# Kernel optimization log

Measured on AMD Instinct MI355X. Metric: run time of the kernel, lower is better.

## Reference

```python
import jax, jax.numpy as jnp
import numpy as np

DIM = 256
B, N, M = 4, 4096, 8


def setup_inputs() -> dict:
    key = jax.random.key(0)
    ks = jax.random.split(key, 12)
    s = 1.0 / np.sqrt(DIM)
    return {
        "q": jax.random.normal(ks[0], (B, DIM, N, M), jnp.float32),
        "k": jax.random.normal(ks[1], (B, DIM, N, M), jnp.float32),
        "pos": jax.random.normal(ks[2], (B, N, M, DIM), jnp.float32),
        "mask": jnp.ones((B, N, M, 1), jnp.int32),
        "Wq": jax.random.normal(ks[3], (DIM, DIM), jnp.float32) * s,
        "Wk": jax.random.normal(ks[4], (DIM, DIM), jnp.float32) * s,
        "Wv": jax.random.normal(ks[5], (DIM, DIM), jnp.float32) * s,
        "W1": jax.random.normal(ks[6], (DIM, DIM // 2), jnp.float32) * s,
        "b1": jnp.zeros((DIM // 2,), jnp.float32),
        "W2": jax.random.normal(ks[7], (DIM // 2, DIM), jnp.float32) * s,
        "b2": jnp.zeros((DIM,), jnp.float32),
        "Wo": jax.random.normal(ks[8], (DIM, DIM), jnp.float32) * s,
        "bo": jnp.zeros((DIM,), jnp.float32),
    }


def reference(q, k, pos, mask, Wq, Wk, Wv, W1, b1, W2, b2, Wo, bo):
    # (B, dim, N, M) -> (B, N, M, dim)
    qh = jnp.einsum('bdnm,de->bnme', q, Wq)
    kh = jnp.einsum('bdnm,de->bnme', k, Wk)
    v = kh @ Wv  # note: v_fc applied to k_fc output, as in the original
    attn = kh - qh + pos
    attn = jax.nn.relu(attn @ W1 + b1) @ W2 + b2
    attn = jnp.where(mask == 0, -1e9, attn)
    attn = jax.nn.sigmoid(attn)
    x = (v + pos) * attn
    x = x @ Wo + bo
    return jnp.transpose(x, (0, 3, 1, 2))  # back to (B, dim, N, M)
```

## Files before the change

kernel.cpp:

```cpp
#include <hip/hip_runtime.h>

#define DIMX 256
#define NMX  32768
#define TB   64
#define PITCH 544

typedef short s16x8 __attribute__((ext_vector_type(8)));
typedef float f32x4 __attribute__((ext_vector_type(4)));

#define OFF_WQN   (0u)
#define OFF_WK    (131072u)
#define OFF_WKV   (262144u)
#define OFF_W1    (393216u)
#define OFF_W2    (458752u)
#define OFF_WO    (524288u)
#define OFF_KVF32 (655360u)

__device__ __forceinline__ ushort f2bf(float f) {
  uint u = __builtin_bit_cast(uint, f);
  return (ushort)((u + 0x7FFFu + ((u >> 16) & 1u)) >> 16);
}

__device__ __forceinline__ uint cvtpk(float lo, float hi) {
  uint r;
  asm("v_cvt_pk_bf16_f32 %0, %1, %2" : "=v"(r) : "v"(lo), "v"(hi));
  return r;
}
__device__ __forceinline__ float bf_lo(uint u) {
  return __builtin_bit_cast(float, u << 16);
}
__device__ __forceinline__ float bf_hi(uint u) {
  return __builtin_bit_cast(float, u & 0xffff0000u);
}

__global__ void wkv_kernel(const float* __restrict__ Wk, const float* __restrict__ Wv,
                           float* __restrict__ outw) {
  const int e = threadIdx.x, d = blockIdx.x;
  float acc = 0.f;
  #pragma unroll 8
  for (int m = 0; m < DIMX; ++m) acc += Wk[d * DIMX + m] * Wv[m * DIMX + e];
  outw[d * DIMX + e] = acc;
}

__global__ void pack_kernel(const float* __restrict__ Wq, const float* __restrict__ Wk,
                            const float* __restrict__ Wkvf, const float* __restrict__ W1,
                            const float* __restrict__ W2, const float* __restrict__ Wo,
                            ushort* __restrict__ wsout) {
  const int fid = blockIdx.x, lane = threadIdx.x;
  const float* src; int Eout = 256; float sgn = 1.f; uint off; int local;
  if (fid < 128)      { src = Wq;   sgn = -1.f; off = OFF_WQN; local = fid;       }
  else if (fid < 256) { src = Wk;   off = OFF_WK;  local = fid - 128;             }
  else if (fid < 384) { src = Wkvf; off = OFF_WKV; local = fid - 256;             }
  else if (fid < 448) { src = W1;   Eout = 128; off = OFF_W1; local = fid - 384;  }
  else if (fid < 512) { src = W2;   off = OFF_W2;  local = fid - 448;             }
  else                { src = Wo;   off = OFF_WO;  local = fid - 512;             }
  const int R  = Eout >> 4;
  const int ks = local / R, r = local - ks * R;
  const int e  = r * 16 + (lane & 15);
  const int k0 = ks * 32 + (lane >> 4) * 8;
  union { uint4 u4; ushort us[8]; } o;
  #pragma unroll
  for (int j = 0; j < 8; ++j) o.us[j] = f2bf(sgn * src[(k0 + j) * Eout + e]);
  *(uint4*)((char*)wsout + off + (((uint)local * 64u + (uint)lane) * 16u)) = o.u4;
}

#define MFMA16(A,B,C) __builtin_amdgcn_mfma_f32_16x16x32_bf16(A, B, C, 0, 0, 0)

__global__ __launch_bounds__(512, 4) void fused_main(
    const float* __restrict__ q, const float* __restrict__ kin,
    const float* __restrict__ pos, const int* __restrict__ mask,
    const float* __restrict__ b1, const float* __restrict__ b2,
    const float* __restrict__ bo, const ushort* __restrict__ wfr,
    float* __restrict__ out)
{
  __shared__ __align__(128) char ba[TB * PITCH];
  __shared__ __align__(128) char bb[TB * PITCH];
  const char* wb = (const char*)wfr;

  const int tid = threadIdx.x;
  const int w = tid >> 6, l = tid & 63;
  const int c = l & 15, g = l >> 4;
  const int b  = blockIdx.x >> 9;
  const int t0 = (blockIdx.x & 511) * TB;

  auto ldB = [&](const char* buf, int ks, int tf) -> s16x8 {
    const int t = (tf << 4) + c;
    const int col = (ks << 6) + (g << 4);
    return *(const s16x8*)(buf + t * PITCH + (col ^ ((t & 7) << 4)));
  };
  auto ldA = [&](uint moff, int fi) -> s16x8 {
    return *(const s16x8*)(wb + moff + (((uint)fi << 6) | (uint)l) * 16u);
  };
  auto stW4 = [&](char* buf, int e0, int t, uint lo, uint hi) {
    const int byte = t * PITCH + (((uint)(e0 * 2)) ^ ((t & 7) << 4));
    *(uint2*)(buf + byte) = uint2{lo, hi};
  };

  const size_t gbase = (size_t)b * DIMX * NMX + t0 + l;

  #pragma unroll
  for (int j4 = 0; j4 < 4; ++j4) {
    const int d0 = (w << 5) + (j4 << 3);
    uint pq[4], pk[4];
    #pragma unroll
    for (int p = 0; p < 4; ++p) {
      const size_t o0 = gbase + (size_t)(d0 + 2 * p) * NMX;
      const size_t o1 = o0 + NMX;
      pq[p] = cvtpk(__builtin_nontemporal_load(q + o0),
                    __builtin_nontemporal_load(q + o1));
      pk[p] = cvtpk(__builtin_nontemporal_load(kin + o0),
                    __builtin_nontemporal_load(kin + o1));
    }
    const int byte = l * PITCH + ((d0 << 1) ^ ((l & 7) << 4));
    *(uint4*)(ba + byte) = uint4{pq[0], pq[1], pq[2], pq[3]};
    *(uint4*)(bb + byte) = uint4{pk[0], pk[1], pk[2], pk[3]};
  }

  f32x4 posr[4][2];
  {
    const float* pz = pos + ((size_t)b * NMX + t0) * DIMX;
    #pragma unroll
    for (int tf = 0; tf < 4; ++tf) {
      const int t = (tf << 4) + c;
      #pragma unroll
      for (int ef = 0; ef < 2; ++ef) {
        const int e0 = (w << 5) + (ef << 4) + (g << 2);
        posr[tf][ef] =
            __builtin_nontemporal_load((const f32x4*)(pz + (size_t)t * DIMX + e0));
      }
    }
  }
  int mk[4];
  #pragma unroll
  for (int tf = 0; tf < 4; ++tf)
    mk[tf] = mask[(size_t)b * NMX + t0 + (tf << 4) + c];

  __syncthreads();

  uint posbf[2][4][2];
  #pragma unroll
  for (int tf = 0; tf < 4; ++tf)
    #pragma unroll
    for (int ef = 0; ef < 2; ++ef) {
      posbf[ef][tf][0] = cvtpk(posr[tf][ef][0], posr[tf][ef][1]);
      posbf[ef][tf][1] = cvtpk(posr[tf][ef][2], posr[tf][ef][3]);
    }

  f32x4 av[2][4], aa[2][4];
  #pragma unroll
  for (int ef = 0; ef < 2; ++ef)
    #pragma unroll
    for (int tf = 0; tf < 4; ++tf) {
      av[ef][tf] = f32x4{0.f, 0.f, 0.f, 0.f};
      aa[ef][tf] = f32x4{0.f, 0.f, 0.f, 0.f};
    }
  #pragma unroll 2
  for (int ks = 0; ks < 8; ++ks) {
    const s16x8 v0 = ldA(OFF_WKV, (ks << 4) + (w << 1));
    const s16x8 v1 = ldA(OFF_WKV, (ks << 4) + (w << 1) + 1);
    const s16x8 k0 = ldA(OFF_WK,  (ks << 4) + (w << 1));
    const s16x8 k1 = ldA(OFF_WK,  (ks << 4) + (w << 1) + 1);
    #pragma unroll
    for (int tf = 0; tf < 4; ++tf) {
      const s16x8 bf = ldB(bb, ks, tf);
      av[0][tf] = MFMA16(v0, bf, av[0][tf]);
      av[1][tf] = MFMA16(v1, bf, av[1][tf]);
      aa[0][tf] = MFMA16(k0, bf, aa[0][tf]);
      aa[1][tf] = MFMA16(k1, bf, aa[1][tf]);
    }
  }
  uint vbf[2][4][2];
  #pragma unroll
  for (int ef = 0; ef < 2; ++ef)
    #pragma unroll
    for (int tf = 0; tf < 4; ++tf) {
      vbf[ef][tf][0] = cvtpk(av[ef][tf][0], av[ef][tf][1]);
      vbf[ef][tf][1] = cvtpk(av[ef][tf][2], av[ef][tf][3]);
    }

  #pragma unroll 2
  for (int ks = 0; ks < 8; ++ks) {
    const s16x8 a0 = ldA(OFF_WQN, (ks << 4) + (w << 1));
    const s16x8 a1 = ldA(OFF_WQN, (ks << 4) + (w << 1) + 1);
    #pragma unroll
    for (int tf = 0; tf < 4; ++tf) {
      const s16x8 bf = ldB(ba, ks, tf);
      aa[0][tf] = MFMA16(a0, bf, aa[0][tf]);
      aa[1][tf] = MFMA16(a1, bf, aa[1][tf]);
    }
  }
  __syncthreads();

  #pragma unroll
  for (int tf = 0; tf < 4; ++tf) {
    const int t = (tf << 4) + c;
    #pragma unroll
    for (int ef = 0; ef < 2; ++ef) {
      const int e0 = (w << 5) + (ef << 4) + (g << 2);
      const uint p0 = posbf[ef][tf][0], p1 = posbf[ef][tf][1];
      const uint lo = cvtpk(aa[ef][tf][0] + bf_lo(p0), aa[ef][tf][1] + bf_hi(p0));
      const uint hi = cvtpk(aa[ef][tf][2] + bf_lo(p1), aa[ef][tf][3] + bf_hi(p1));
      stW4(ba, e0, t, lo, hi);
    }
  }
  __syncthreads();

  f32x4 ah[4];
  #pragma unroll
  for (int tf = 0; tf < 4; ++tf) ah[tf] = f32x4{0.f, 0.f, 0.f, 0.f};
  #pragma unroll 2
  for (int ks = 0; ks < 8; ++ks) {
    const s16x8 a0 = ldA(OFF_W1, (ks << 3) + w);
    #pragma unroll
    for (int tf = 0; tf < 4; ++tf) {
      const s16x8 bf = ldB(ba, ks, tf);
      ah[tf] = MFMA16(a0, bf, ah[tf]);
    }
  }
  {
    const int e0h = (w << 4) + (g << 2);
    const f32x4 b1v = *(const f32x4*)(b1 + e0h);
    #pragma unroll
    for (int tf = 0; tf < 4; ++tf) {
      const int t = (tf << 4) + c;
      const uint lo = cvtpk(fmaxf(ah[tf][0] + b1v[0], 0.f),
                            fmaxf(ah[tf][1] + b1v[1], 0.f));
      const uint hi = cvtpk(fmaxf(ah[tf][2] + b1v[2], 0.f),
                            fmaxf(ah[tf][3] + b1v[3], 0.f));
      stW4(bb, e0h, t, lo, hi);
    }
  }
  __syncthreads();

  f32x4 as_[2][4];
  #pragma unroll
  for (int ef = 0; ef < 2; ++ef)
    #pragma unroll
    for (int tf = 0; tf < 4; ++tf) as_[ef][tf] = f32x4{0.f, 0.f, 0.f, 0.f};
  #pragma unroll
  for (int ks = 0; ks < 4; ++ks) {
    const s16x8 a0 = ldA(OFF_W2, (ks << 4) + (w << 1));
    const s16x8 a1 = ldA(OFF_W2, (ks << 4) + (w << 1) + 1);
    #pragma unroll
    for (int tf = 0; tf < 4; ++tf) {
      const s16x8 bf = ldB(bb, ks, tf);
      as_[0][tf] = MFMA16(a0, bf, as_[0][tf]);
      as_[1][tf] = MFMA16(a1, bf, as_[1][tf]);
    }
  }
  #pragma unroll
  for (int tf = 0; tf < 4; ++tf) {
    const int t = (tf << 4) + c;
    #pragma unroll
    for (int ef = 0; ef < 2; ++ef) {
      const int e0 = (w << 5) + (ef << 4) + (g << 2);
      const f32x4 b2v = *(const f32x4*)(b2 + e0);
      float xv[4];
      #pragma unroll
      for (int i = 0; i < 4; ++i) {
        float sv = as_[ef][tf][i] + b2v[i];
        if (mk[tf] == 0) sv = -1e9f;
        const float sig = 1.f / (1.f + __expf(-sv));
        const uint pv = vbf[ef][tf][i >> 1];
        const uint pp = posbf[ef][tf][i >> 1];
        const float vv = (i & 1) ? bf_hi(pv) : bf_lo(pv);
        const float pf = (i & 1) ? bf_hi(pp) : bf_lo(pp);
        xv[i] = (vv + pf) * sig;
      }
      stW4(ba, e0, t, cvtpk(xv[0], xv[1]), cvtpk(xv[2], xv[3]));
    }
  }
  __syncthreads();

  f32x4 ao[2][4];
  #pragma unroll
  for (int ef = 0; ef < 2; ++ef)
    #pragma unroll
    for (int tf = 0; tf < 4; ++tf) ao[ef][tf] = f32x4{0.f, 0.f, 0.f, 0.f};
  #pragma unroll 2
  for (int ks = 0; ks < 8; ++ks) {
    const s16x8 a0 = ldA(OFF_WO, (ks << 4) + (w << 1));
    const s16x8 a1 = ldA(OFF_WO, (ks << 4) + (w << 1) + 1);
    #pragma unroll
    for (int tf = 0; tf < 4; ++tf) {
      const s16x8 bf = ldB(ba, ks, tf);
      ao[0][tf] = MFMA16(a0, bf, ao[0][tf]);
      ao[1][tf] = MFMA16(a1, bf, ao[1][tf]);
    }
  }
  #pragma unroll
  for (int ef = 0; ef < 2; ++ef) {
    const int e0 = (w << 5) + (ef << 4) + (g << 2);
    const f32x4 bov = *(const f32x4*)(bo + e0);
    #pragma unroll
    for (int i = 0; i < 4; ++i) {
      float* ob = out + ((size_t)b * DIMX + e0 + i) * NMX + t0 + c;
      #pragma unroll
      for (int tf = 0; tf < 4; ++tf)
        ob[tf << 4] = ao[ef][tf][i] + bov[i];
    }
  }
}

extern "C" void kernel_launch(void* const* d_in, const int* in_sizes, int n_in,
                              void* d_out, int out_size, void* d_ws, size_t ws_size,
                              hipStream_t stream) {
  (void)in_sizes; (void)n_in; (void)out_size; (void)ws_size;
  const float* q   = (const float*)d_in[0];
  const float* k   = (const float*)d_in[1];
  const float* pos = (const float*)d_in[2];
  const int*   msk = (const int*)d_in[3];
  const float* Wq  = (const float*)d_in[4];
  const float* Wk  = (const float*)d_in[5];
  const float* Wv  = (const float*)d_in[6];
  const float* W1  = (const float*)d_in[7];
  const float* b1  = (const float*)d_in[8];
  const float* W2  = (const float*)d_in[9];
  const float* b2  = (const float*)d_in[10];
  const float* Wo  = (const float*)d_in[11];
  const float* bo  = (const float*)d_in[12];
  float* out = (float*)d_out;
  char* ws = (char*)d_ws;
  float*  wkvf = (float*)(ws + OFF_KVF32);
  ushort* wfr  = (ushort*)ws;

  wkv_kernel<<<dim3(256), dim3(256), 0, stream>>>(Wk, Wv, wkvf);
  pack_kernel<<<dim3(640), dim3(64), 0, stream>>>(Wq, Wk, wkvf, W1, W2, Wo, wfr);
  fused_main<<<dim3(2048), dim3(512), 0, stream>>>(q, k, pos, msk, b1, b2, bo, wfr, out);
}
```

Measured before the change: 180.7 us.

## Shrink LDS by staging q in two halves through a half-width buffer

Replaces the second full-width LDS tile with a half-width one (APITCH 288) so the block's shared memory drops from about 68KB to about 53KB. The q tile is loaded in two halves: the upper half is held in registers, written into the small buffer after the first half's MFMAs, and consumed in a second K loop. The W1 hidden output (128 wide) also reuses the small buffer. The launch-bounds min-blocks hint rises from 4 to 6 to allow more resident blocks, at the cost of an extra barrier, extra live registers for the held q values, and tighter register limits.

```diff
diff --git a/kernel.cpp b/kernel.cpp
--- a/kernel.cpp
+++ b/kernel.cpp
@@ -4,6 +4,7 @@
 #define NMX  32768
 #define TB   64
 #define PITCH 544
+#define APITCH 288
 
 typedef short s16x8 __attribute__((ext_vector_type(8)));
 typedef float f32x4 __attribute__((ext_vector_type(4)));
@@ -66,15 +67,15 @@
 
 #define MFMA16(A,B,C) __builtin_amdgcn_mfma_f32_16x16x32_bf16(A, B, C, 0, 0, 0)
 
-__global__ __launch_bounds__(512, 4) void fused_main(
+__global__ __launch_bounds__(512, 6) void fused_main(
     const float* __restrict__ q, const float* __restrict__ kin,
     const float* __restrict__ pos, const int* __restrict__ mask,
     const float* __restrict__ b1, const float* __restrict__ b2,
     const float* __restrict__ bo, const ushort* __restrict__ wfr,
     float* __restrict__ out)
 {
-  __shared__ __align__(128) char ba[TB * PITCH];
-  __shared__ __align__(128) char bb[TB * PITCH];
+  __shared__ __align__(128) char mb[TB * PITCH];
+  __shared__ __align__(128) char ab[TB * APITCH];
   const char* wb = (const char*)wfr;
 
   const int tid = threadIdx.x;
@@ -83,17 +84,26 @@
   const int b  = blockIdx.x >> 9;
   const int t0 = (blockIdx.x & 511) * TB;
 
-  auto ldB = [&](const char* buf, int ks, int tf) -> s16x8 {
+  auto ldBm = [&](int ks, int tf) -> s16x8 {
     const int t = (tf << 4) + c;
     const int col = (ks << 6) + (g << 4);
-    return *(const s16x8*)(buf + t * PITCH + (col ^ ((t & 7) << 4)));
+    return *(const s16x8*)(mb + t * PITCH + (col ^ ((t & 7) << 4)));
+  };
+  auto ldBa = [&](int ks, int tf) -> s16x8 {
+    const int t = (tf << 4) + c;
+    const int col = (ks << 6) + (g << 4);
+    return *(const s16x8*)(ab + t * APITCH + (col ^ ((t & 7) << 4)));
   };
   auto ldA = [&](uint moff, int fi) -> s16x8 {
     return *(const s16x8*)(wb + moff + (((uint)fi << 6) | (uint)l) * 16u);
   };
-  auto stW4 = [&](char* buf, int e0, int t, uint lo, uint hi) {
+  auto stM4 = [&](int e0, int t, uint lo, uint hi) {
     const int byte = t * PITCH + (((uint)(e0 * 2)) ^ ((t & 7) << 4));
-    *(uint2*)(buf + byte) = uint2{lo, hi};
+    *(uint2*)(mb + byte) = uint2{lo, hi};
+  };
+  auto stA4 = [&](int e0, int t, uint lo, uint hi) {
+    const int byte = t * APITCH + (((uint)(e0 * 2)) ^ ((t & 7) << 4));
+    *(uint2*)(ab + byte) = uint2{lo, hi};
   };
 
   const size_t gbase = (size_t)b * DIMX * NMX + t0 + l;
@@ -101,19 +111,39 @@
   #pragma unroll
   for (int j4 = 0; j4 < 4; ++j4) {
     const int d0 = (w << 5) + (j4 << 3);
-    uint pq[4], pk[4];
+    uint pk[4];
     #pragma unroll
     for (int p = 0; p < 4; ++p) {
       const size_t o0 = gbase + (size_t)(d0 + 2 * p) * NMX;
-      const size_t o1 = o0 + NMX;
+      pk[p] = cvtpk(__builtin_nontemporal_load(kin + o0),
+                    __builtin_nontemporal_load(kin + o0 + NMX));
+    }
+    const int byte = l * PITCH + ((d0 << 1) ^ ((l & 7) << 4));
+    *(uint4*)(mb + byte) = uint4{pk[0], pk[1], pk[2], pk[3]};
+  }
+  #pragma unroll
+  for (int j4 = 0; j4 < 2; ++j4) {
+    const int dl = (w << 4) + (j4 << 3);
+    uint pq[4];
+    #pragma unroll
+    for (int p = 0; p < 4; ++p) {
+      const size_t o0 = gbase + (size_t)(dl + 2 * p) * NMX;
       pq[p] = cvtpk(__builtin_nontemporal_load(q + o0),
-                    __builtin_nontemporal_load(q + o1));
-      pk[p] = cvtpk(__builtin_nontemporal_load(kin + o0),
-                    __builtin_nontemporal_load(kin + o1));
-    }
-    const int byte = l * PITCH + ((d0 << 1) ^ ((l & 7) << 4));
-    *(uint4*)(ba + byte) = uint4{pq[0], pq[1], pq[2], pq[3]};
-    *(uint4*)(bb + byte) = uint4{pk[0], pk[1], pk[2], pk[3]};
+                    __builtin_nontemporal_load(q + o0 + NMX));
+    }
+    const int byte = l * APITCH + ((dl << 1) ^ ((l & 7) << 4));
+    *(uint4*)(ab + byte) = uint4{pq[0], pq[1], pq[2], pq[3]};
+  }
+  uint qh[8];
+  #pragma unroll
+  for (int j4 = 0; j4 < 2; ++j4) {
+    const int d = 128 + (w << 4) + (j4 << 3);
+    #pragma unroll
+    for (int p = 0; p < 4; ++p) {
+      const size_t o0 = gbase + (size_t)(d + 2 * p) * NMX;
+      qh[j4 * 4 + p] = cvtpk(__builtin_nontemporal_load(q + o0),
+                             __builtin_nontemporal_load(q + o0 + NMX));
+    }
   }
 
   f32x4 posr[4][2];
@@ -162,7 +192,7 @@
     const s16x8 k1 = ldA(OFF_WK,  (ks << 4) + (w << 1) + 1);
     #pragma unroll
     for (int tf = 0; tf < 4; ++tf) {
-      const s16x8 bf = ldB(bb, ks, tf);
+      const s16x8 bf = ldBm(ks, tf);
       av[0][tf] = MFMA16(v0, bf, av[0][tf]);
       av[1][tf] = MFMA16(v1, bf, av[1][tf]);
       aa[0][tf] = MFMA16(k0, bf, aa[0][tf]);
@@ -179,17 +209,38 @@
     }
 
   #pragma unroll 2
-  for (int ks = 0; ks < 8; ++ks) {
+  for (int ks = 0; ks < 4; ++ks) {
     const s16x8 a0 = ldA(OFF_WQN, (ks << 4) + (w << 1));
     const s16x8 a1 = ldA(OFF_WQN, (ks << 4) + (w << 1) + 1);
     #pragma unroll
     for (int tf = 0; tf < 4; ++tf) {
-      const s16x8 bf = ldB(ba, ks, tf);
+      const s16x8 bf = ldBa(ks, tf);
       aa[0][tf] = MFMA16(a0, bf, aa[0][tf]);
       aa[1][tf] = MFMA16(a1, bf, aa[1][tf]);
     }
   }
   __syncthreads();
+
+  #pragma unroll
+  for (int j4 = 0; j4 < 2; ++j4) {
+    const int dl = (w << 4) + (j4 << 3);
+    const int byte = l * APITCH + ((dl << 1) ^ ((l & 7) << 4));
+    *(uint4*)(ab + byte) = uint4{qh[j4 * 4], qh[j4 * 4 + 1],
+                                 qh[j4 * 4 + 2], qh[j4 * 4 + 3]};
+  }
+  __syncthreads();
+
+  #pragma unroll 2
+  for (int ks = 4; ks < 8; ++ks) {
+    const s16x8 a0 = ldA(OFF_WQN, (ks << 4) + (w << 1));
+    const s16x8 a1 = ldA(OFF_WQN, (ks << 4) + (w << 1) + 1);
+    #pragma unroll
+    for (int tf = 0; tf < 4; ++tf) {
+      const s16x8 bf = ldBa(ks - 4, tf);
+      aa[0][tf] = MFMA16(a0, bf, aa[0][tf]);
+      aa[1][tf] = MFMA16(a1, bf, aa[1][tf]);
+    }
+  }
 
   #pragma unroll
   for (int tf = 0; tf < 4; ++tf) {
@@ -200,7 +251,7 @@
       const uint p0 = posbf[ef][tf][0], p1 = posbf[ef][tf][1];
       const uint lo = cvtpk(aa[ef][tf][0] + bf_lo(p0), aa[ef][tf][1] + bf_hi(p0));
       const uint hi = cvtpk(aa[ef][tf][2] + bf_lo(p1), aa[ef][tf][3] + bf_hi(p1));
-      stW4(ba, e0, t, lo, hi);
+      stM4(e0, t, lo, hi);
     }
   }
   __syncthreads();
@@ -213,7 +264,7 @@
     const s16x8 a0 = ldA(OFF_W1, (ks << 3) + w);
     #pragma unroll
     for (int tf = 0; tf < 4; ++tf) {
-      const s16x8 bf = ldB(ba, ks, tf);
+      const s16x8 bf = ldBm(ks, tf);
       ah[tf] = MFMA16(a0, bf, ah[tf]);
     }
   }
@@ -227,7 +278,7 @@
                             fmaxf(ah[tf][1] + b1v[1], 0.f));
       const uint hi = cvtpk(fmaxf(ah[tf][2] + b1v[2], 0.f),
                             fmaxf(ah[tf][3] + b1v[3], 0.f));
-      stW4(bb, e0h, t, lo, hi);
+      stA4(e0h, t, lo, hi);
     }
   }
   __syncthreads();
@@ -243,7 +294,7 @@
     const s16x8 a1 = ldA(OFF_W2, (ks << 4) + (w << 1) + 1);
     #pragma unroll
     for (int tf = 0; tf < 4; ++tf) {
-      const s16x8 bf = ldB(bb, ks, tf);
+      const s16x8 bf = ldBa(ks, tf);
       as_[0][tf] = MFMA16(a0, bf, as_[0][tf]);
       as_[1][tf] = MFMA16(a1, bf, as_[1][tf]);
     }
@@ -267,7 +318,7 @@
         const float pf = (i & 1) ? bf_hi(pp) : bf_lo(pp);
         xv[i] = (vv + pf) * sig;
       }
-      stW4(ba, e0, t, cvtpk(xv[0], xv[1]), cvtpk(xv[2], xv[3]));
+      stM4(e0, t, cvtpk(xv[0], xv[1]), cvtpk(xv[2], xv[3]));
     }
   }
   __syncthreads();
@@ -283,7 +334,7 @@
     const s16x8 a1 = ldA(OFF_WO, (ks << 4) + (w << 1) + 1);
     #pragma unroll
     for (int tf = 0; tf < 4; ++tf) {
-      const s16x8 bf = ldB(ba, ks, tf);
+      const s16x8 bf = ldBm(ks, tf);
       ao[0][tf] = MFMA16(a0, bf, ao[0][tf]);
       ao[1][tf] = MFMA16(a1, bf, ao[1][tf]);
     }
```

Result: slower. 450.2 us (+149.2%).

## Switch 256-wide GEMM stages from 16x16x32 to 32x32x16 bf16 MFMA

Applied to the files above, without the earlier changes.

Re-lays out the packed weight fragments for the 256-output matrices and rewrites the K/V, Q, W2 and Wo stages to use 32x32x16 MFMA tiles with 32-token fragments instead of 16x16x32 tiles. This halves the number of MFMA instructions and A-fragment loads per stage and changes the per-lane accumulator layout, so the pos, mask and epilogue indexing are adapted. The W1 stage keeps 16x16 tiles. Larger accumulators may raise register pressure under the 512x4 launch bounds, and the new LDS read pattern may change bank-conflict behaviour.

```diff
diff --git a/kernel.cpp b/kernel.cpp
--- a/kernel.cpp
+++ b/kernel.cpp
@@ -7,6 +7,7 @@
 
 typedef short s16x8 __attribute__((ext_vector_type(8)));
 typedef float f32x4 __attribute__((ext_vector_type(4)));
+typedef float f32x16 __attribute__((ext_vector_type(16)));
 
 #define OFF_WQN   (0u)
 #define OFF_WK    (131072u)
@@ -20,7 +21,6 @@
   uint u = __builtin_bit_cast(uint, f);
   return (ushort)((u + 0x7FFFu + ((u >> 16) & 1u)) >> 16);
 }
-
 __device__ __forceinline__ uint cvtpk(float lo, float hi) {
   uint r;
   asm("v_cvt_pk_bf16_f32 %0, %1, %2" : "=v"(r) : "v"(lo), "v"(hi));
@@ -47,17 +47,17 @@
                             const float* __restrict__ W2, const float* __restrict__ Wo,
                             ushort* __restrict__ wsout) {
   const int fid = blockIdx.x, lane = threadIdx.x;
-  const float* src; int Eout = 256; float sgn = 1.f; uint off; int local;
+  const float* src; int Eout = 256; float sgn = 1.f; uint off; int local; int m32 = 1;
   if (fid < 128)      { src = Wq;   sgn = -1.f; off = OFF_WQN; local = fid;       }
   else if (fid < 256) { src = Wk;   off = OFF_WK;  local = fid - 128;             }
   else if (fid < 384) { src = Wkvf; off = OFF_WKV; local = fid - 256;             }
-  else if (fid < 448) { src = W1;   Eout = 128; off = OFF_W1; local = fid - 384;  }
+  else if (fid < 448) { src = W1;   Eout = 128; m32 = 0; off = OFF_W1; local = fid - 384; }
   else if (fid < 512) { src = W2;   off = OFF_W2;  local = fid - 448;             }
   else                { src = Wo;   off = OFF_WO;  local = fid - 512;             }
-  const int R  = Eout >> 4;
-  const int ks = local / R, r = local - ks * R;
-  const int e  = r * 16 + (lane & 15);
-  const int k0 = ks * 32 + (lane >> 4) * 8;
+  const int ks = local >> 3, r = local & 7;
+  int e, k0;
+  if (m32) { e = r * 32 + (lane & 31); k0 = ks * 16 + (lane >> 5) * 8; }
+  else     { e = r * 16 + (lane & 15); k0 = ks * 32 + (lane >> 4) * 8; }
   union { uint4 u4; ushort us[8]; } o;
   #pragma unroll
   for (int j = 0; j < 8; ++j) o.us[j] = f2bf(sgn * src[(k0 + j) * Eout + e]);
@@ -65,6 +65,7 @@
 }
 
 #define MFMA16(A,B,C) __builtin_amdgcn_mfma_f32_16x16x32_bf16(A, B, C, 0, 0, 0)
+#define MFMA32(A,B,C) __builtin_amdgcn_mfma_f32_32x32x16_bf16(A, B, C, 0, 0, 0)
 
 __global__ __launch_bounds__(512, 4) void fused_main(
     const float* __restrict__ q, const float* __restrict__ kin,
@@ -80,10 +81,16 @@
   const int tid = threadIdx.x;
   const int w = tid >> 6, l = tid & 63;
   const int c = l & 15, g = l >> 4;
+  const int tl = l & 31, h2 = l >> 5;
   const int b  = blockIdx.x >> 9;
   const int t0 = (blockIdx.x & 511) * TB;
 
-  auto ldB = [&](const char* buf, int ks, int tf) -> s16x8 {
+  auto ldB32 = [&](const char* buf, int ks, int tf) -> s16x8 {
+    const int t = (tf << 5) + tl;
+    const int col = (ks << 5) + (h2 << 4);
+    return *(const s16x8*)(buf + t * PITCH + (col ^ ((t & 7) << 4)));
+  };
+  auto ldB16 = [&](const char* buf, int ks, int tf) -> s16x8 {
     const int t = (tf << 4) + c;
     const int col = (ks << 6) + (g << 4);
     return *(const s16x8*)(buf + t * PITCH + (col ^ ((t & 7) << 4)));
@@ -116,90 +123,81 @@
     *(uint4*)(bb + byte) = uint4{pk[0], pk[1], pk[2], pk[3]};
   }
 
-  f32x4 posr[4][2];
+  f32x4 posr[2][4];
   {
     const float* pz = pos + ((size_t)b * NMX + t0) * DIMX;
     #pragma unroll
-    for (int tf = 0; tf < 4; ++tf) {
-      const int t = (tf << 4) + c;
+    for (int tf = 0; tf < 2; ++tf) {
+      const int t = (tf << 5) + tl;
       #pragma unroll
-      for (int ef = 0; ef < 2; ++ef) {
-        const int e0 = (w << 5) + (ef << 4) + (g << 2);
-        posr[tf][ef] =
+      for (int a = 0; a < 4; ++a) {
+        const int e0 = (w << 5) + (a << 3) + (h2 << 2);
+        posr[tf][a] =
             __builtin_nontemporal_load((const f32x4*)(pz + (size_t)t * DIMX + e0));
       }
     }
   }
-  int mk[4];
-  #pragma unroll
-  for (int tf = 0; tf < 4; ++tf)
-    mk[tf] = mask[(size_t)b * NMX + t0 + (tf << 4) + c];
-
-  __syncthreads();
-
-  uint posbf[2][4][2];
-  #pragma unroll
-  for (int tf = 0; tf < 4; ++tf)
-    #pragma unroll
-    for (int ef = 0; ef < 2; ++ef) {
-      posbf[ef][tf][0] = cvtpk(posr[tf][ef][0], posr[tf][ef][1]);
-      posbf[ef][tf][1] = cvtpk(posr[tf][ef][2], posr[tf][ef][3]);
-    }
-
-  f32x4 av[2][4], aa[2][4];
-  #pragma unroll
-  for (int ef = 0; ef < 2; ++ef)
-    #pragma unroll
-    for (int tf = 0; tf < 4; ++tf) {
-      av[ef][tf] = f32x4{0.f, 0.f, 0.f, 0.f};
-      aa[ef][tf] = f32x4{0.f, 0.f, 0.f, 0.f};
-    }
-  #pragma unroll 2
-  for (int ks = 0; ks < 8; ++ks) {
-    const s16x8 v0 = ldA(OFF_WKV, (ks << 4) + (w << 1));
-    const s16x8 v1 = ldA(OFF_WKV, (ks << 4) + (w << 1) + 1);
-    const s16x8 k0 = ldA(OFF_WK,  (ks << 4) + (w << 1));
-    const s16x8 k1 = ldA(OFF_WK,  (ks << 4) + (w << 1) + 1);
-    #pragma unroll
-    for (int tf = 0; tf < 4; ++tf) {
-      const s16x8 bf = ldB(bb, ks, tf);
-      av[0][tf] = MFMA16(v0, bf, av[0][tf]);
-      av[1][tf] = MFMA16(v1, bf, av[1][tf]);
-      aa[0][tf] = MFMA16(k0, bf, aa[0][tf]);
-      aa[1][tf] = MFMA16(k1, bf, aa[1][tf]);
-    }
-  }
-  uint vbf[2][4][2];
-  #pragma unroll
-  for (int ef = 0; ef < 2; ++ef)
-    #pragma unroll
-    for (int tf = 0; tf < 4; ++tf) {
-      vbf[ef][tf][0] = cvtpk(av[ef][tf][0], av[ef][tf][1]);
-      vbf[ef][tf][1] = cvtpk(av[ef][tf][2], av[ef][tf][3]);
-    }
-
-  #pragma unroll 2
-  for (int ks = 0; ks < 8; ++ks) {
-    const s16x8 a0 = ldA(OFF_WQN, (ks << 4) + (w << 1));
-    const s16x8 a1 = ldA(OFF_WQN, (ks << 4) + (w << 1) + 1);
-    #pragma unroll
-    for (int tf = 0; tf < 4; ++tf) {
-      const s16x8 bf = ldB(ba, ks, tf);
-      aa[0][tf] = MFMA16(a0, bf, aa[0][tf]);
-      aa[1][tf] = MFMA16(a1, bf, aa[1][tf]);
-    }
-  }
-  __syncthreads();
-
-  #pragma unroll
-  for (int tf = 0; tf < 4; ++tf) {
-    const int t = (tf << 4) + c;
-    #pragma unroll
-    for (int ef = 0; ef < 2; ++ef) {
-      const int e0 = (w << 5) + (ef << 4) + (g << 2);
-      const uint p0 = posbf[ef][tf][0], p1 = posbf[ef][tf][1];
-      const uint lo = cvtpk(aa[ef][tf][0] + bf_lo(p0), aa[ef][tf][1] + bf_hi(p0));
-      const uint hi = cvtpk(aa[ef][tf][2] + bf_lo(p1), aa[ef][tf][3] + bf_hi(p1));
+  int mk[2];
+  #pragma unroll
+  for (int tf = 0; tf < 2; ++tf)
+    mk[tf] = mask[(size_t)b * NMX + t0 + (tf << 5) + tl];
+
+  __syncthreads();
+
+  uint posbf[2][8];
+  #pragma unroll
+  for (int tf = 0; tf < 2; ++tf)
+    #pragma unroll
+    for (int a = 0; a < 4; ++a) {
+      posbf[tf][2 * a]     = cvtpk(posr[tf][a][0], posr[tf][a][1]);
+      posbf[tf][2 * a + 1] = cvtpk(posr[tf][a][2], posr[tf][a][3]);
+    }
+
+  f32x16 av[2], aa[2];
+  #pragma unroll
+  for (int tf = 0; tf < 2; ++tf)
+    #pragma unroll
+    for (int i = 0; i < 16; ++i) { av[tf][i] = 0.f; aa[tf][i] = 0.f; }
+  #pragma unroll 2
+  for (int ks = 0; ks < 16; ++ks) {
+    const s16x8 v0 = ldA(OFF_WKV, (ks << 3) + w);
+    const s16x8 k0 = ldA(OFF_WK,  (ks << 3) + w);
+    #pragma unroll
+    for (int tf = 0; tf < 2; ++tf) {
+      const s16x8 bf = ldB32(bb, ks, tf);
+      av[tf] = MFMA32(v0, bf, av[tf]);
+      aa[tf] = MFMA32(k0, bf, aa[tf]);
+    }
+  }
+  uint vbf[2][8];
+  #pragma unroll
+  for (int tf = 0; tf < 2; ++tf)
+    #pragma unroll
+    for (int p = 0; p < 8; ++p)
+      vbf[tf][p] = cvtpk(av[tf][2 * p], av[tf][2 * p + 1]);
+
+  #pragma unroll 2
+  for (int ks = 0; ks < 16; ++ks) {
+    const s16x8 a0 = ldA(OFF_WQN, (ks << 3) + w);
+    #pragma unroll
+    for (int tf = 0; tf < 2; ++tf) {
+      const s16x8 bf = ldB32(ba, ks, tf);
+      aa[tf] = MFMA32(a0, bf, aa[tf]);
+    }
+  }
+  __syncthreads();
+
+  #pragma unroll
+  for (int tf = 0; tf < 2; ++tf) {
+    const int t = (tf << 5) + tl;
+    #pragma unroll
+    for (int a = 0; a < 4; ++a) {
+      const int e0 = (w << 5) + (a << 3) + (h2 << 2);
+      const uint p0 = posbf[tf][2 * a], p1 = posbf[tf][2 * a + 1];
+      const uint lo = cvtpk(aa[tf][4 * a + 0] + bf_lo(p0),
+                            aa[tf][4 * a + 1] + bf_hi(p0));
+      const uint hi = cvtpk(aa[tf][4 * a + 2] + bf_lo(p1),
+                            aa[tf][4 * a + 3] + bf_hi(p1));
       stW4(ba, e0, t, lo, hi);
     }
   }
@@ -213,7 +211,7 @@
     const s16x8 a0 = ldA(OFF_W1, (ks << 3) + w);
     #pragma unroll
     for (int tf = 0; tf < 4; ++tf) {
-      const s16x8 bf = ldB(ba, ks, tf);
+      const s16x8 bf = ldB16(ba, ks, tf);
       ah[tf] = MFMA16(a0, bf, ah[tf]);
     }
   }
@@ -232,72 +230,68 @@
   }
   __syncthreads();
 
-  f32x4 as_[2][4];
-  #pragma unroll
-  for (int ef = 0; ef < 2; ++ef)
-    #pragma unroll
-    for (int tf = 0; tf < 4; ++tf) as_[ef][tf] = f32x4{0.f, 0.f, 0.f, 0.f};
-  #pragma unroll
-  for (int ks = 0; ks < 4; ++ks) {
-    const s16x8 a0 = ldA(OFF_W2, (ks << 4) + (w << 1));
-    const s16x8 a1 = ldA(OFF_W2, (ks << 4) + (w << 1) + 1);
-    #pragma unroll
-    for (int tf = 0; tf < 4; ++tf) {
-      const s16x8 bf = ldB(bb, ks, tf);
-      as_[0][tf] = MFMA16(a0, bf, as_[0][tf]);
-      as_[1][tf] = MFMA16(a1, bf, as_[1][tf]);
-    }
-  }
-  #pragma unroll
-  for (int tf = 0; tf < 4; ++tf) {
-    const int t = (tf << 4) + c;
-    #pragma unroll
-    for (int ef = 0; ef < 2; ++ef) {
-      const int e0 = (w << 5) + (ef << 4) + (g << 2);
+  f32x16 as_[2];
+  #pragma unroll
+  for (int tf = 0; tf < 2; ++tf)
+    #pragma unroll
+    for (int i = 0; i < 16; ++i) as_[tf][i] = 0.f;
+  #pragma unroll 2
+  for (int ks = 0; ks < 8; ++ks) {
+    const s16x8 a0 = ldA(OFF_W2, (ks << 3) + w);
+    #pragma unroll
+    for (int tf = 0; tf < 2; ++tf) {
+      const s16x8 bf = ldB32(bb, ks, tf);
+      as_[tf] = MFMA32(a0, bf, as_[tf]);
+    }
+  }
+  #pragma unroll
+  for (int tf = 0; tf < 2; ++tf) {
+    const int t = (tf << 5) + tl;
+    #pragma unroll
+    for (int a = 0; a < 4; ++a) {
+      const int e0 = (w << 5) + (a << 3) + (h2 << 2);
       const f32x4 b2v = *(const f32x4*)(b2 + e0);
       float xv[4];
       #pragma unroll
-      for (int i = 0; i < 4; ++i) {
-        float sv = as_[ef][tf][i] + b2v[i];
+      for (int bq = 0; bq < 4; ++bq) {
+        float sv = as_[tf][4 * a + bq] + b2v[bq];
         if (mk[tf] == 0) sv = -1e9f;
         const float sig = 1.f / (1.f + __expf(-sv));
-        const uint pv = vbf[ef][tf][i >> 1];
-        const uint pp = posbf[ef][tf][i >> 1];
-        const float vv = (i & 1) ? bf_hi(pv) : bf_lo(pv);
-        const float pf = (i & 1) ? bf_hi(pp) : bf_lo(pp);
-        xv[i] = (vv + pf) * sig;
+        const uint pv = vbf[tf][2 * a + (bq >> 1)];
+        const uint pp = posbf[tf][2 * a + (bq >> 1)];
+        const float vv = (bq & 1) ? bf_hi(pv) : bf_lo(pv);
+        const float pf = (bq & 1) ? bf_hi(pp) : bf_lo(pp);
+        xv[bq] = (vv + pf) * sig;
       }
       stW4(ba, e0, t, cvtpk(xv[0], xv[1]), cvtpk(xv[2], xv[3]));
     }
   }
   __syncthreads();
 
-  f32x4 ao[2][4];
-  #pragma unroll
-  for (int ef = 0; ef < 2; ++ef)
-    #pragma unroll
-    for (int tf = 0; tf < 4; ++tf) ao[ef][tf] = f32x4{0.f, 0.f, 0.f, 0.f};
-  #pragma unroll 2
-  for (int ks = 0; ks < 8; ++ks) {
-    const s16x8 a0 = ldA(OFF_WO, (ks << 4) + (w << 1));
-    const s16x8 a1 = ldA(OFF_WO, (ks << 4) + (w << 1) + 1);
-    #pragma unroll
-    for (int tf = 0; tf < 4; ++tf) {
-      const s16x8 bf = ldB(ba, ks, tf);
-      ao[0][tf] = MFMA16(a0, bf, ao[0][tf]);
-      ao[1][tf] = MFMA16(a1, bf, ao[1][tf]);
-    }
-  }
-  #pragma unroll
-  for (int ef = 0; ef < 2; ++ef) {
-    const int e0 = (w << 5) + (ef << 4) + (g << 2);
-    const f32x4 bov = *(const f32x4*)(bo + e0);
-    #pragma unroll
-    for (int i = 0; i < 4; ++i) {
-      float* ob = out + ((size_t)b * DIMX + e0 + i) * NMX + t0 + c;
+  f32x16 ao[2];
+  #pragma unroll
+  for (int tf = 0; tf < 2; ++tf)
+    #pragma unroll
+    for (int i = 0; i < 16; ++i) ao[tf][i] = 0.f;
+  #pragma unroll 2
+  for (int ks = 0; ks < 16; ++ks) {
+    const s16x8 a0 = ldA(OFF_WO, (ks << 3) + w);
+    #pragma unroll
+    for (int tf = 0; tf < 2; ++tf) {
+      const s16x8 bf = ldB32(ba, ks, tf);
+      ao[tf] = MFMA32(a0, bf, ao[tf]);
+    }
+  }
+  #pragma unroll
+  for (int tf = 0; tf < 2; ++tf) {
+    const int t = t0 + (tf << 5) + tl;
+    #pragma unroll
+    for (int a = 0; a < 4; ++a) {
+      const int e0 = (w << 5) + (a << 3) + (h2 << 2);
+      const f32x4 bov = *(const f32x4*)(bo + e0);
       #pragma unroll
-      for (int tf = 0; tf < 4; ++tf)
-        ob[tf << 4] = ao[ef][tf][i] + bov[i];
+      for (int bq = 0; bq < 4; ++bq)
+        out[((size_t)b * DIMX + e0 + bq) * NMX + t] = ao[tf][4 * a + bq] + bov[bq];
     }
   }
 }
```

Result: slower. 197.9 us (+9.5%).

## Make fused kernel persistent over four tiles with register prefetch of next q/k

Applied to the files above, without the earlier changes.

Each block now handles four consecutive 64-token tiles, so the grid is 512 blocks instead of 2048. The next tile's k and q are loaded into registers during the W1 and Wo GEMM phases and stored to LDS at the start of the next iteration, to hide global load latency behind MFMA work. The Wq and Wk/Wkv projection loops are also merged into one k-loop. The costs are higher register pressure (64 prefetch floats), which may reduce occupancy under launch_bounds(512,4), and fewer blocks than before to fill the GPU's CUs.

```diff
diff --git a/kernel.cpp b/kernel.cpp
--- a/kernel.cpp
+++ b/kernel.cpp
@@ -20,7 +20,6 @@
   uint u = __builtin_bit_cast(uint, f);
   return (ushort)((u + 0x7FFFu + ((u >> 16) & 1u)) >> 16);
 }
-
 __device__ __forceinline__ uint cvtpk(float lo, float hi) {
   uint r;
   asm("v_cvt_pk_bf16_f32 %0, %1, %2" : "=v"(r) : "v"(lo), "v"(hi));
@@ -80,8 +79,8 @@
   const int tid = threadIdx.x;
   const int w = tid >> 6, l = tid & 63;
   const int c = l & 15, g = l >> 4;
-  const int b  = blockIdx.x >> 9;
-  const int t0 = (blockIdx.x & 511) * TB;
+  const int b  = blockIdx.x >> 7;
+  const int t0base = (blockIdx.x & 127) * 256;
 
   auto ldB = [&](const char* buf, int ks, int tf) -> s16x8 {
     const int t = (tf << 4) + c;
@@ -96,209 +95,253 @@
     *(uint2*)(buf + byte) = uint2{lo, hi};
   };
 
-  const size_t gbase = (size_t)b * DIMX * NMX + t0 + l;
-
-  #pragma unroll
-  for (int j4 = 0; j4 < 4; ++j4) {
-    const int d0 = (w << 5) + (j4 << 3);
-    uint pq[4], pk[4];
-    #pragma unroll
-    for (int p = 0; p < 4; ++p) {
-      const size_t o0 = gbase + (size_t)(d0 + 2 * p) * NMX;
-      const size_t o1 = o0 + NMX;
-      pq[p] = cvtpk(__builtin_nontemporal_load(q + o0),
-                    __builtin_nontemporal_load(q + o1));
-      pk[p] = cvtpk(__builtin_nontemporal_load(kin + o0),
-                    __builtin_nontemporal_load(kin + o1));
-    }
-    const int byte = l * PITCH + ((d0 << 1) ^ ((l & 7) << 4));
-    *(uint4*)(ba + byte) = uint4{pq[0], pq[1], pq[2], pq[3]};
-    *(uint4*)(bb + byte) = uint4{pk[0], pk[1], pk[2], pk[3]};
-  }
-
-  f32x4 posr[4][2];
-  {
-    const float* pz = pos + ((size_t)b * NMX + t0) * DIMX;
+  uint qn[16], kn[16];
+
+  #pragma unroll 1
+  for (int it = 0; it < 4; ++it) {
+    const int t0 = t0base + (it << 6);
+    const size_t gbase = (size_t)b * DIMX * NMX + t0 + l;
+
+    if (it == 0) {
+      #pragma unroll
+      for (int j4 = 0; j4 < 4; ++j4) {
+        const int d0 = (w << 5) + (j4 << 3);
+        uint pq[4], pk[4];
+        #pragma unroll
+        for (int p = 0; p < 4; ++p) {
+          const size_t o0 = gbase + (size_t)(d0 + 2 * p) * NMX;
+          const size_t o1 = o0 + NMX;
+          pq[p] = cvtpk(__builtin_nontemporal_load(q + o0),
+                        __builtin_nontemporal_load(q + o1));
+          pk[p] = cvtpk(__builtin_nontemporal_load(kin + o0),
+                        __builtin_nontemporal_load(kin + o1));
+        }
+        const int byte = l * PITCH + ((d0 << 1) ^ ((l & 7) << 4));
+        *(uint4*)(ba + byte) = uint4{pq[0], pq[1], pq[2], pq[3]};
+        *(uint4*)(bb + byte) = uint4{pk[0], pk[1], pk[2], pk[3]};
+      }
+    } else {
+      #pragma unroll
+      for (int j4 = 0; j4 < 4; ++j4) {
+        const int d0 = (w << 5) + (j4 << 3);
+        const int byte = l * PITCH + ((d0 << 1) ^ ((l & 7) << 4));
+        *(uint4*)(ba + byte) = uint4{qn[4*j4], qn[4*j4+1], qn[4*j4+2], qn[4*j4+3]};
+        *(uint4*)(bb + byte) = uint4{kn[4*j4], kn[4*j4+1], kn[4*j4+2], kn[4*j4+3]};
+      }
+    }
+
+    f32x4 posr[4][2];
+    {
+      const float* pz = pos + ((size_t)b * NMX + t0) * DIMX;
+      #pragma unroll
+      for (int tf = 0; tf < 4; ++tf) {
+        const int t = (tf << 4) + c;
+        #pragma unroll
+        for (int ef = 0; ef < 2; ++ef) {
+          const int e0 = (w << 5) + (ef << 4) + (g << 2);
+          posr[tf][ef] =
+              __builtin_nontemporal_load((const f32x4*)(pz + (size_t)t * DIMX + e0));
+        }
+      }
+    }
+    int mk[4];
+    #pragma unroll
+    for (int tf = 0; tf < 4; ++tf)
+      mk[tf] = mask[(size_t)b * NMX + t0 + (tf << 4) + c];
+
+    __syncthreads();
+
+    uint posbf[2][4][2];
+    #pragma unroll
+    for (int tf = 0; tf < 4; ++tf)
+      #pragma unroll
+      for (int ef = 0; ef < 2; ++ef) {
+        posbf[ef][tf][0] = cvtpk(posr[tf][ef][0], posr[tf][ef][1]);
+        posbf[ef][tf][1] = cvtpk(posr[tf][ef][2], posr[tf][ef][3]);
+      }
+
+    f32x4 av[2][4], aa[2][4];
+    #pragma unroll
+    for (int ef = 0; ef < 2; ++ef)
+      #pragma unroll
+      for (int tf = 0; tf < 4; ++tf) {
+        av[ef][tf] = f32x4{0.f, 0.f, 0.f, 0.f};
+        aa[ef][tf] = f32x4{0.f, 0.f, 0.f, 0.f};
+      }
+    #pragma unroll 2
+    for (int ks = 0; ks < 8; ++ks) {
+      const s16x8 v0 = ldA(OFF_WKV, (ks << 4) + (w << 1));
+      const s16x8 v1 = ldA(OFF_WKV, (ks << 4) + (w << 1) + 1);
+      const s16x8 k0 = ldA(OFF_WK,  (ks << 4) + (w << 1));
+      const s16x8 k1 = ldA(OFF_WK,  (ks << 4) + (w << 1) + 1);
+      const s16x8 a0 = ldA(OFF_WQN, (ks << 4) + (w << 1));
+      const s16x8 a1 = ldA(OFF_WQN, (ks << 4) + (w << 1) + 1);
+      #pragma unroll
+      for (int tf = 0; tf < 4; ++tf) {
+        const s16x8 bk = ldB(bb, ks, tf);
+        const s16x8 bq = ldB(ba, ks, tf);
+        av[0][tf] = MFMA16(v0, bk, av[0][tf]);
+        av[1][tf] = MFMA16(v1, bk, av[1][tf]);
+        aa[0][tf] = MFMA16(k0, bk, aa[0][tf]);
+        aa[1][tf] = MFMA16(k1, bk, aa[1][tf]);
+        aa[0][tf] = MFMA16(a0, bq, aa[0][tf]);
+        aa[1][tf] = MFMA16(a1, bq, aa[1][tf]);
+      }
+    }
+    uint vbf[2][4][2];
+    #pragma unroll
+    for (int ef = 0; ef < 2; ++ef)
+      #pragma unroll
+      for (int tf = 0; tf < 4; ++tf) {
+        vbf[ef][tf][0] = cvtpk(av[ef][tf][0], av[ef][tf][1]);
+        vbf[ef][tf][1] = cvtpk(av[ef][tf][2], av[ef][tf][3]);
+      }
+    __syncthreads();
+
     #pragma unroll
     for (int tf = 0; tf < 4; ++tf) {
       const int t = (tf << 4) + c;
       #pragma unroll
       for (int ef = 0; ef < 2; ++ef) {
         const int e0 = (w << 5) + (ef << 4) + (g << 2);
-        posr[tf][ef] =
-            __builtin_nontemporal_load((const f32x4*)(pz + (size_t)t * DIMX + e0));
-      }
-    }
-  }
-  int mk[4];
-  #pragma unroll
-  for (int tf = 0; tf < 4; ++tf)
-    mk[tf] = mask[(size_t)b * NMX + t0 + (tf << 4) + c];
-
-  __syncthreads();
-
-  uint posbf[2][4][2];
-  #pragma unroll
-  for (int tf = 0; tf < 4; ++tf)
-    #pragma unroll
-    for (int ef = 0; ef < 2; ++ef) {
-      posbf[ef][tf][0] = cvtpk(posr[tf][ef][0], posr[tf][ef][1]);
-      posbf[ef][tf][1] = cvtpk(posr[tf][ef][2], posr[tf][ef][3]);
-    }
-
-  f32x4 av[2][4], aa[2][4];
-  #pragma unroll
-  for (int ef = 0; ef < 2; ++ef)
+        const uint p0 = posbf[ef][tf][0], p1 = posbf[ef][tf][1];
+        const uint lo = cvtpk(aa[ef][tf][0] + bf_lo(p0), aa[ef][tf][1] + bf_hi(p0));
+        const uint hi = cvtpk(aa[ef][tf][2] + bf_lo(p1), aa[ef][tf][3] + bf_hi(p1));
+        stW4(ba, e0, t, lo, hi);
+      }
+    }
+    __syncthreads();
+
+    float kf[32];
+    if (it < 3) {
+      #pragma unroll
+      for (int j4 = 0; j4 < 4; ++j4) {
+        const int d0 = (w << 5) + (j4 << 3);
+        #pragma unroll
+        for (int p = 0; p < 4; ++p) {
+          const size_t o0 = gbase + 64 + (size_t)(d0 + 2 * p) * NMX;
+          kf[j4 * 8 + 2 * p]     = __builtin_nontemporal_load(kin + o0);
+          kf[j4 * 8 + 2 * p + 1] = __builtin_nontemporal_load(kin + o0 + NMX);
+        }
+      }
+    }
+    f32x4 ah[4];
+    #pragma unroll
+    for (int tf = 0; tf < 4; ++tf) ah[tf] = f32x4{0.f, 0.f, 0.f, 0.f};
+    #pragma unroll 2
+    for (int ks = 0; ks < 8; ++ks) {
+      const s16x8 a0 = ldA(OFF_W1, (ks << 3) + w);
+      #pragma unroll
+      for (int tf = 0; tf < 4; ++tf) {
+        const s16x8 bf = ldB(ba, ks, tf);
+        ah[tf] = MFMA16(a0, bf, ah[tf]);
+      }
+    }
+    if (it < 3) {
+      #pragma unroll
+      for (int i = 0; i < 16; ++i) kn[i] = cvtpk(kf[2 * i], kf[2 * i + 1]);
+    }
+    {
+      const int e0h = (w << 4) + (g << 2);
+      const f32x4 b1v = *(const f32x4*)(b1 + e0h);
+      #pragma unroll
+      for (int tf = 0; tf < 4; ++tf) {
+        const int t = (tf << 4) + c;
+        const uint lo = cvtpk(fmaxf(ah[tf][0] + b1v[0], 0.f),
+                              fmaxf(ah[tf][1] + b1v[1], 0.f));
+        const uint hi = cvtpk(fmaxf(ah[tf][2] + b1v[2], 0.f),
+                              fmaxf(ah[tf][3] + b1v[3], 0.f));
+        stW4(bb, e0h, t, lo, hi);
+      }
+    }
+    __syncthreads();
+
+    f32x4 as_[2][4];
+    #pragma unroll
+    for (int ef = 0; ef < 2; ++ef)
+      #pragma unroll
+      for (int tf = 0; tf < 4; ++tf) as_[ef][tf] = f32x4{0.f, 0.f, 0.f, 0.f};
+    #pragma unroll
+    for (int ks = 0; ks < 4; ++ks) {
+      const s16x8 a0 = ldA(OFF_W2, (ks << 4) + (w << 1));
+      const s16x8 a1 = ldA(OFF_W2, (ks << 4) + (w << 1) + 1);
+      #pragma unroll
+      for (int tf = 0; tf < 4; ++tf) {
+        const s16x8 bf = ldB(bb, ks, tf);
+        as_[0][tf] = MFMA16(a0, bf, as_[0][tf]);
+        as_[1][tf] = MFMA16(a1, bf, as_[1][tf]);
+      }
+    }
     #pragma unroll
     for (int tf = 0; tf < 4; ++tf) {
-      av[ef][tf] = f32x4{0.f, 0.f, 0.f, 0.f};
-      aa[ef][tf] = f32x4{0.f, 0.f, 0.f, 0.f};
-    }
-  #pragma unroll 2
-  for (int ks = 0; ks < 8; ++ks) {
-    const s16x8 v0 = ldA(OFF_WKV, (ks << 4) + (w << 1));
-    const s16x8 v1 = ldA(OFF_WKV, (ks << 4) + (w << 1) + 1);
-    const s16x8 k0 = ldA(OFF_WK,  (ks << 4) + (w << 1));
-    const s16x8 k1 = ldA(OFF_WK,  (ks << 4) + (w << 1) + 1);
-    #pragma unroll
-    for (int tf = 0; tf < 4; ++tf) {
-      const s16x8 bf = ldB(bb, ks, tf);
-      av[0][tf] = MFMA16(v0, bf, av[0][tf]);
-      av[1][tf] = MFMA16(v1, bf, av[1][tf]);
-      aa[0][tf] = MFMA16(k0, bf, aa[0][tf]);
-      aa[1][tf] = MFMA16(k1, bf, aa[1][tf]);
-    }
-  }
-  uint vbf[2][4][2];
-  #pragma unroll
-  for (int ef = 0; ef < 2; ++ef)
-    #pragma unroll
-    for (int tf = 0; tf < 4; ++tf) {
-      vbf[ef][tf][0] = cvtpk(av[ef][tf][0], av[ef][tf][1]);
-      vbf[ef][tf][1] = cvtpk(av[ef][tf][2], av[ef][tf][3]);
-    }
-
-  #pragma unroll 2
-  for (int ks = 0; ks < 8; ++ks) {
-    const s16x8 a0 = ldA(OFF_WQN, (ks << 4) + (w << 1));
-    const s16x8 a1 = ldA(OFF_WQN, (ks << 4) + (w << 1) + 1);
-    #pragma unroll
-    for (int tf = 0; tf < 4; ++tf) {
-      const s16x8 bf = ldB(ba, ks, tf);
-      aa[0][tf] = MFMA16(a0, bf, aa[0][tf]);
-      aa[1][tf] = MFMA16(a1, bf, aa[1][tf]);
-    }
-  }
-  __syncthreads();
-
-  #pragma unroll
-  for (int tf = 0; tf < 4; ++tf) {
-    const int t = (tf << 4) + c;
+      const int t = (tf << 4) + c;
+      #pragma unroll
+      for (int ef = 0; ef < 2; ++ef) {
+        const int e0 = (w << 5) + (ef << 4) + (g << 2);
+        const f32x4 b2v = *(const f32x4*)(b2 + e0);
+        float xv[4];
+        #pragma unroll
+        for (int i = 0; i < 4; ++i) {
+          float sv = as_[ef][tf][i] + b2v[i];
+          if (mk[tf] == 0) sv = -1e9f;
+          const float sig = 1.f / (1.f + __expf(-sv));
+          const uint pv = vbf[ef][tf][i >> 1];
+          const uint pp = posbf[ef][tf][i >> 1];
+          const float vv = (i & 1) ? bf_hi(pv) : bf_lo(pv);
+          const float pf = (i & 1) ? bf_hi(pp) : bf_lo(pp);
+          xv[i] = (vv + pf) * sig;
+        }
+        stW4(ba, e0, t, cvtpk(xv[0], xv[1]), cvtpk(xv[2], xv[3]));
+      }
+    }
+    __syncthreads();
+
+    float qf[32];
+    if (it < 3) {
+      #pragma unroll
+      for (int j4 = 0; j4 < 4; ++j4) {
+        const int d0 = (w << 5) + (j4 << 3);
+        #pragma unroll
+        for (int p = 0; p < 4; ++p) {
+          const size_t o0 = gbase + 64 + (size_t)(d0 + 2 * p) * NMX;
+          qf[j4 * 8 + 2 * p]     = __builtin_nontemporal_load(q + o0);
+          qf[j4 * 8 + 2 * p + 1] = __builtin_nontemporal_load(q + o0 + NMX);
+        }
+      }
+    }
+    f32x4 ao[2][4];
+    #pragma unroll
+    for (int ef = 0; ef < 2; ++ef)
+      #pragma unroll
+      for (int tf = 0; tf < 4; ++tf) ao[ef][tf] = f32x4{0.f, 0.f, 0.f, 0.f};
+    #pragma unroll 2
+    for (int ks = 0; ks < 8; ++ks) {
+      const s16x8 a0 = ldA(OFF_WO, (ks << 4) + (w << 1));
+      const s16x8 a1 = ldA(OFF_WO, (ks << 4) + (w << 1) + 1);
+      #pragma unroll
+      for (int tf = 0; tf < 4; ++tf) {
+        const s16x8 bf = ldB(ba, ks, tf);
+        ao[0][tf] = MFMA16(a0, bf, ao[0][tf]);
+        ao[1][tf] = MFMA16(a1, bf, ao[1][tf]);
+      }
+    }
+    if (it < 3) {
+      #pragma unroll
+      for (int i = 0; i < 16; ++i) qn[i] = cvtpk(qf[2 * i], qf[2 * i + 1]);
+    }
     #pragma unroll
     for (int ef = 0; ef < 2; ++ef) {
       const int e0 = (w << 5) + (ef << 4) + (g << 2);
-      const uint p0 = posbf[ef][tf][0], p1 = posbf[ef][tf][1];
-      const uint lo = cvtpk(aa[ef][tf][0] + bf_lo(p0), aa[ef][tf][1] + bf_hi(p0));
-      const uint hi = cvtpk(aa[ef][tf][2] + bf_lo(p1), aa[ef][tf][3] + bf_hi(p1));
-      stW4(ba, e0, t, lo, hi);
-    }
-  }
-  __syncthreads();
-
-  f32x4 ah[4];
-  #pragma unroll
-  for (int tf = 0; tf < 4; ++tf) ah[tf] = f32x4{0.f, 0.f, 0.f, 0.f};
-  #pragma unroll 2
-  for (int ks = 0; ks < 8; ++ks) {
-    const s16x8 a0 = ldA(OFF_W1, (ks << 3) + w);
-    #pragma unroll
-    for (int tf = 0; tf < 4; ++tf) {
-      const s16x8 bf = ldB(ba, ks, tf);
-      ah[tf] = MFMA16(a0, bf, ah[tf]);
-    }
-  }
-  {
-    const int e0h = (w << 4) + (g << 2);
-    const f32x4 b1v = *(const f32x4*)(b1 + e0h);
-    #pragma unroll
-    for (int tf = 0; tf < 4; ++tf) {
-      const int t = (tf << 4) + c;
-      const uint lo = cvtpk(fmaxf(ah[tf][0] + b1v[0], 0.f),
-                            fmaxf(ah[tf][1] + b1v[1], 0.f));
-      const uint hi = cvtpk(fmaxf(ah[tf][2] + b1v[2], 0.f),
-                            fmaxf(ah[tf][3] + b1v[3], 0.f));
-      stW4(bb, e0h, t, lo, hi);
-    }
-  }
-  __syncthreads();
-
-  f32x4 as_[2][4];
-  #pragma unroll
-  for (int ef = 0; ef < 2; ++ef)
-    #pragma unroll
-    for (int tf = 0; tf < 4; ++tf) as_[ef][tf] = f32x4{0.f, 0.f, 0.f, 0.f};
-  #pragma unroll
-  for (int ks = 0; ks < 4; ++ks) {
-    const s16x8 a0 = ldA(OFF_W2, (ks << 4) + (w << 1));
-    const s16x8 a1 = ldA(OFF_W2, (ks << 4) + (w << 1) + 1);
-    #pragma unroll
-    for (int tf = 0; tf < 4; ++tf) {
-      const s16x8 bf = ldB(bb, ks, tf);
-      as_[0][tf] = MFMA16(a0, bf, as_[0][tf]);
-      as_[1][tf] = MFMA16(a1, bf, as_[1][tf]);
-    }
-  }
-  #pragma unroll
-  for (int tf = 0; tf < 4; ++tf) {
-    const int t = (tf << 4) + c;
-    #pragma unroll
-    for (int ef = 0; ef < 2; ++ef) {
-      const int e0 = (w << 5) + (ef << 4) + (g << 2);
-      const f32x4 b2v = *(const f32x4*)(b2 + e0);
-      float xv[4];
+      const f32x4 bov = *(const f32x4*)(bo + e0);
       #pragma unroll
       for (int i = 0; i < 4; ++i) {
-        float sv = as_[ef][tf][i] + b2v[i];
-        if (mk[tf] == 0) sv = -1e9f;
-        const float sig = 1.f / (1.f + __expf(-sv));
-        const uint pv = vbf[ef][tf][i >> 1];
-        const uint pp = posbf[ef][tf][i >> 1];
-        const float vv = (i & 1) ? bf_hi(pv) : bf_lo(pv);
-        const float pf = (i & 1) ? bf_hi(pp) : bf_lo(pp);
-        xv[i] = (vv + pf) * sig;
-      }
-      stW4(ba, e0, t, cvtpk(xv[0], xv[1]), cvtpk(xv[2], xv[3]));
-    }
-  }
-  __syncthreads();
-
-  f32x4 ao[2][4];
-  #pragma unroll
-  for (int ef = 0; ef < 2; ++ef)
-    #pragma unroll
-    for (int tf = 0; tf < 4; ++tf) ao[ef][tf] = f32x4{0.f, 0.f, 0.f, 0.f};
-  #pragma unroll 2
-  for (int ks = 0; ks < 8; ++ks) {
-    const s16x8 a0 = ldA(OFF_WO, (ks << 4) + (w << 1));
-    const s16x8 a1 = ldA(OFF_WO, (ks << 4) + (w << 1) + 1);
-    #pragma unroll
-    for (int tf = 0; tf < 4; ++tf) {
-      const s16x8 bf = ldB(ba, ks, tf);
-      ao[0][tf] = MFMA16(a0, bf, ao[0][tf]);
-      ao[1][tf] = MFMA16(a1, bf, ao[1][tf]);
-    }
-  }
-  #pragma unroll
-  for (int ef = 0; ef < 2; ++ef) {
-    const int e0 = (w << 5) + (ef << 4) + (g << 2);
-    const f32x4 bov = *(const f32x4*)(bo + e0);
-    #pragma unroll
-    for (int i = 0; i < 4; ++i) {
-      float* ob = out + ((size_t)b * DIMX + e0 + i) * NMX + t0 + c;
-      #pragma unroll
-      for (int tf = 0; tf < 4; ++tf)
-        ob[tf << 4] = ao[ef][tf][i] + bov[i];
-    }
+        float* ob = out + ((size_t)b * DIMX + e0 + i) * NMX + t0 + c;
+        #pragma unroll
+        for (int tf = 0; tf < 4; ++tf)
+          ob[tf << 4] = ao[ef][tf][i] + bov[i];
+      }
+    }
+    if (it < 3) __syncthreads();
   }
 }
 
@@ -326,5 +369,5 @@
 
   wkv_kernel<<<dim3(256), dim3(256), 0, stream>>>(Wk, Wv, wkvf);
   pack_kernel<<<dim3(640), dim3(64), 0, stream>>>(Wq, Wk, wkvf, W1, W2, Wo, wfr);
-  fused_main<<<dim3(2048), dim3(512), 0, stream>>>(q, k, pos, msk, b1, b2, bo, wfr, out);
-}
+  fused_main<<<dim3(512), dim3(512), 0, stream>>>(q, k, pos, msk, b1, b2, bo, wfr, out);
+}
```

Measured after the change: 453.6 us. +151.0%, slower.
